# Optimization experiments

Hardware: AMD Instinct MI355X
Metric: run time of the kernel (lower is better)

## Reference

```python
import jax, jax.numpy as jnp
import numpy as np

B, H, S, D = 2, 16, 2048, 128
BS = 128  # block_size
NB = S // BS  # num_blocks
SPARSITY_PROB = 0.5


def setup_inputs() -> dict:
    key = jax.random.key(0)
    kq, kk, kv, km = jax.random.split(key, 4)
    query = jax.random.normal(kq, (B, H, S, D), dtype=jnp.float32)
    k_ = jax.random.normal(kk, (B, H, S, D), dtype=jnp.float32)
    v_ = jax.random.normal(kv, (B, H, S, D), dtype=jnp.float32)
    # block pattern: rand < sparsity_prob, diagonal forced True (causal=False)
    block_mask = jax.random.uniform(km, (NB, NB)) < SPARSITY_PROB
    block_mask = block_mask | jnp.eye(NB, dtype=bool)
    return {"query": query, "key": k_, "value": v_,
            "block_mask": block_mask, "block_size": BS}


def reference(query, key, value, block_mask, block_size):
    b, h, s, d = query.shape
    nb = s // block_size
    scale = 1.0 / jnp.sqrt(jnp.float32(d))
    # reshape into blocks: (b, h, nb, bs, d)
    qb = query.reshape(b, h, nb, block_size, d)
    kb = key.reshape(b, h, nb, block_size, d)
    vb = value.reshape(b, h, nb, block_size, d)
    # per-(i,j)-block scores: (b, h, i, j, q, k)
    scores = jnp.einsum('bhiqd,bhjkd->bhijqk', qb, kb) * scale
    # IMPORTANT: softmax is taken independently within each block (axis=-1),
    # matching the original's per-block (non-merged) softmax.
    attn = jax.nn.softmax(scores, axis=-1)
    # zero out inactive blocks, then sum contributions over j
    attn = attn * block_mask[None, None, :, :, None, None].astype(attn.dtype)
    out = jnp.einsum('bhijqk,bhjkd->bhiqd', attn, vb)
    return out.reshape(b, h, s, d)
```

## Files before the change

### kernel.cpp

```cpp
#include <hip/hip_runtime.h>
#include <stdint.h>

#define CBDIM 256
#define WBDIM 256
#define DBDIM 512

#if __has_builtin(__builtin_amdgcn_permlane32_swap) && \
    __has_builtin(__builtin_amdgcn_permlane16_swap)
#define HAVE_PERMLANE_SWAP 1
#else
#define HAVE_PERMLANE_SWAP 0
#endif

typedef __attribute__((ext_vector_type(8))) short short8;
typedef __attribute__((ext_vector_type(4))) float f32x4;

__device__ __forceinline__ unsigned f2bf(float f) {
    union { float f; unsigned u; } a; a.f = f;
    unsigned r = a.u + 0x7fffu + ((a.u >> 16) & 1u);
    return (r >> 16) & 0xffffu;
}
__device__ __forceinline__ float f4e(float4 v, int e) {
    return e == 0 ? v.x : e == 1 ? v.y : e == 2 ? v.z : v.w;
}
__device__ __forceinline__ unsigned u4e(uint4 v, int e) {
    return e == 0 ? v.x : e == 1 ? v.y : e == 2 ? v.z : v.w;
}
__device__ __forceinline__ uint2 shfl_u2(uint2 v, int src) {
    uint2 r;
    r.x = (unsigned)__shfl((int)v.x, src);
    r.y = (unsigned)__shfl((int)v.y, src);
    return r;
}
__device__ __forceinline__ bool detect_bf16(const void* p) {
    unsigned w = ((const unsigned*)p)[threadIdx.x & 63];
    unsigned lo = w & 0xffffu, ex = (lo >> 7) & 0xffu;
    bool pl = (lo == 0u) || (ex >= 0x68u && ex <= 0x86u);
    return __popcll(__ballot(pl)) >= 40;
}
__device__ __forceinline__ void gload_lds16(const void* g, void* l) {
    __builtin_amdgcn_global_load_lds(
        (const __attribute__((address_space(1))) void*)g,
        (__attribute__((address_space(3))) void*)l, 16, 0, 0);
}

__global__ __launch_bounds__(CBDIM)
void convert_kswz(const void* __restrict__ src, uint4* __restrict__ dst, int nIds)
{
    bool isBf = detect_bf16(src);
    int stride = gridDim.x * CBDIM;
    for (int id = blockIdx.x * CBDIM + threadIdx.x; id < nIds; id += stride) {
        int lid = id & 2047, tt = id >> 11;
        int r = lid >> 4, c = (lid & 15) ^ (r & 7);
        size_t eo = (size_t)tt * 16384 + (size_t)r * 128 + c * 8;
        uint4 w;
        if (isBf) {
            w = *(const uint4*)((const unsigned short*)src + eo);
        } else {
            const float* p = (const float*)src + eo;
            float4 f0 = *(const float4*)p, f1 = *(const float4*)(p + 4);
            w.x = f2bf(f0.x) | (f2bf(f0.y) << 16);
            w.y = f2bf(f0.z) | (f2bf(f0.w) << 16);
            w.z = f2bf(f1.x) | (f2bf(f1.y) << 16);
            w.w = f2bf(f1.z) | (f2bf(f1.w) << 16);
        }
        dst[id] = w;
    }
}

__global__ __launch_bounds__(CBDIM)
void convert_vt(const void* __restrict__ src, uint4* __restrict__ dst,
                const unsigned char* __restrict__ Mb, int* __restrict__ order)
{
    __shared__ unsigned short lv[16384];
    const int tid = threadIdx.x, t = blockIdx.x;
    bool isBf = detect_bf16(src);

    if (t == 0 && tid < 64) {
        int tt = tid;
        unsigned mu = ((const unsigned*)Mb)[tt];
        bool maskByte = (__ballot((mu & 0xFFFFFF00u) != 0u) != 0ull);
        int cnt = 0;
        if (tt < 16)
            for (int j = 0; j < 16; ++j) {
                bool a = maskByte ? (Mb[tt * 16 + j] != 0)
                                  : (((const int*)Mb)[tt * 16 + j] != 0);
                cnt += a ? 1 : 0;
            }
        int rank = 0;
        for (int j = 0; j < 16; ++j) {
            int cj = __shfl(cnt, j);
            if (cj > cnt || (cj == cnt && j < tt)) ++rank;
        }
        if (tt < 16) order[rank] = tt;
    }

    size_t ebase = (size_t)t * 16384;
    if (isBf) {
#pragma unroll
        for (int it = 0; it < 8; ++it) {
            int id = it * CBDIM + tid;
            *(uint4*)&lv[id * 8] = ((const uint4*)src)[ebase / 8 + id];
        }
    } else {
#pragma unroll
        for (int it = 0; it < 16; ++it) {
            int f = it * CBDIM + tid;
            float4 v = ((const float4*)src)[ebase / 4 + f];
            uint2 pk;
            pk.x = f2bf(v.x) | (f2bf(v.y) << 16);
            pk.y = f2bf(v.z) | (f2bf(v.w) << 16);
            *(uint2*)&lv[f * 4] = pk;
        }
    }
    __syncthreads();
#pragma unroll
    for (int it = 0; it < 8; ++it) {
        int id = it * CBDIM + tid;
        int d = id >> 4, c = (id & 15) ^ (d & 7);
        const unsigned short* col = &lv[(size_t)(c * 8) * 128 + d];
        uint4 w;
        w.x = col[0]   | ((unsigned)col[128] << 16);
        w.y = col[256] | ((unsigned)col[384] << 16);
        w.z = col[512] | ((unsigned)col[640] << 16);
        w.w = col[768] | ((unsigned)col[896] << 16);
        dst[(size_t)t * 2048 + id] = w;
    }
}

template<bool QF32>
__device__ __forceinline__ void attn_core(const void* Qv, const uint4* Kw,
                                          const uint4* Vt, unsigned actm,
                                          void* Ov, char* ldsK, char* ldsV,
                                          int bh, int i)
{
    constexpr int S = 2048, D = 128;
    const int tid  = threadIdx.x;
    const int lane = tid & 63;
    const int wv   = tid >> 6;
    const int quad = lane >> 4;
    const int l16  = lane & 15;

    const int qb0 = wv * 32;
    const size_t qrowbase = ((size_t)bh * S + (size_t)i * 128) * D;

    short8 qf[2][4];
#pragma unroll
    for (int nt = 0; nt < 2; ++nt) {
        int qrow = qb0 + nt * 16 + l16;
#pragma unroll
        for (int ks = 0; ks < 4; ++ks) {
            int dof = ks * 32 + quad * 8;
            if constexpr (QF32) {
                const float* qp = (const float*)Qv + qrowbase + (size_t)qrow * D + dof;
                float4 f0 = *(const float4*)qp;
                float4 f1 = *(const float4*)(qp + 4);
                short8 v;
                v[0] = (short)f2bf(f0.x); v[1] = (short)f2bf(f0.y);
                v[2] = (short)f2bf(f0.z); v[3] = (short)f2bf(f0.w);
                v[4] = (short)f2bf(f1.x); v[5] = (short)f2bf(f1.y);
                v[6] = (short)f2bf(f1.z); v[7] = (short)f2bf(f1.w);
                qf[nt][ks] = v;
            } else {
                qf[nt][ks] = *(const short8*)((const unsigned short*)Qv
                              + qrowbase + (size_t)qrow * D + dof);
            }
        }
    }

    f32x4 accO[2][8];
#pragma unroll
    for (int a = 0; a < 2; ++a)
#pragma unroll
        for (int b = 0; b < 8; ++b)
            accO[a][b] = (f32x4){0.f, 0.f, 0.f, 0.f};

    const float C2 = 0.08838834764831845f * 1.44269504088896f;

    auto STAGE = [&](const uint4* t, char* lds) {
#pragma unroll
        for (int it = 0; it < 8; ++it) {
            int id = it * WBDIM + tid;
            int lo = (it * WBDIM + wv * 64) * 16;
            gload_lds16(t + id, lds + lo);
        }
        asm volatile("" ::: "memory");
    };
    auto ktile = [&](int jj) { return Kw + (size_t)(bh * 16 + jj) * 2048; };
    auto vtile = [&](int jj) { return Vt + (size_t)(bh * 16 + jj) * 2048; };

    int j = (int)__builtin_ctz(actm);
    unsigned m = actm & (actm - 1);

    STAGE(ktile(j), ldsK);
    STAGE(vtile(j), ldsV);
    asm volatile("s_waitcnt vmcnt(8)" ::: "memory");
    __syncthreads();

    while (true) {
        int jn = m ? (int)__builtin_ctz(m) : -1;
        if (jn >= 0) m &= m - 1;

        f32x4 accS[2][8];
#pragma unroll
        for (int nt = 0; nt < 2; ++nt)
#pragma unroll
            for (int mt = 0; mt < 8; ++mt)
                accS[nt][mt] = (f32x4){0.f, 0.f, 0.f, 0.f};

#pragma unroll
        for (int mt = 0; mt < 8; ++mt) {
            int r = mt * 16 + l16;
            short8 kf[4];
#pragma unroll
            for (int ks = 0; ks < 4; ++ks) {
                int c = ks * 4 + quad;
                kf[ks] = *(const short8*)(ldsK + r * 256 + ((c ^ (r & 7)) << 4));
            }
            __builtin_amdgcn_s_setprio(1);
#pragma unroll
            for (int nt = 0; nt < 2; ++nt)
#pragma unroll
                for (int ks = 0; ks < 4; ++ks)
                    accS[nt][mt] = __builtin_amdgcn_mfma_f32_16x16x32_bf16(
                        kf[ks], qf[nt][ks], accS[nt][mt], 0, 0, 0);
            __builtin_amdgcn_s_setprio(0);
        }

        uint2 p2[2][8];
#pragma unroll
        for (int nt = 0; nt < 2; ++nt) {
            float ps[8];
#pragma unroll
            for (int mt = 0; mt < 8; ++mt) {
                f32x4 p;
#pragma unroll
                for (int rr = 0; rr < 4; ++rr)
                    p[rr] = exp2f(accS[nt][mt][rr] * C2);
                accS[nt][mt] = p;
                ps[mt] = (p[0] + p[1]) + (p[2] + p[3]);
            }
            float sum = ((ps[0] + ps[1]) + (ps[2] + ps[3]))
                      + ((ps[4] + ps[5]) + (ps[6] + ps[7]));
            sum += __shfl_xor(sum, 16);
            sum += __shfl_xor(sum, 32);
            float rinv = 1.0f / sum;
#pragma unroll
            for (int mt = 0; mt < 8; ++mt) {
                p2[nt][mt].x = f2bf(accS[nt][mt][0] * rinv)
                             | (f2bf(accS[nt][mt][1] * rinv) << 16);
                p2[nt][mt].y = f2bf(accS[nt][mt][2] * rinv)
                             | (f2bf(accS[nt][mt][3] * rinv) << 16);
            }
        }

        asm volatile("s_waitcnt vmcnt(0)" ::: "memory");
        __syncthreads();
        if (jn >= 0) STAGE(ktile(jn), ldsK);

#pragma unroll
        for (int ks = 0; ks < 4; ++ks) {
            short8 pf[2];
#pragma unroll
            for (int nt = 0; nt < 2; ++nt) {
#if HAVE_PERMLANE_SWAP
                unsigned ax = p2[nt][2 * ks + 0].x, ay = p2[nt][2 * ks + 0].y;
                unsigned bx = p2[nt][2 * ks + 1].x, by = p2[nt][2 * ks + 1].y;
                auto rx = __builtin_amdgcn_permlane32_swap(ax, bx, false, false);
                auto ry = __builtin_amdgcn_permlane32_swap(ay, by, false, false);
                auto sx = __builtin_amdgcn_permlane16_swap(rx[0], rx[1], false, false);
                auto sy = __builtin_amdgcn_permlane16_swap(ry[0], ry[1], false, false);
                union { uint4 u; short8 s; } w;
                w.u.x = sx[0]; w.u.y = sy[0]; w.u.z = sx[1]; w.u.w = sy[1];
                pf[nt] = w.s;
#else
                const int srcA = l16 + ((quad & 1) << 5);
                const int srcB = srcA + 16;
                const bool hiMs = (quad >> 1) != 0;
                uint2 a0 = shfl_u2(p2[nt][2 * ks + 0], srcA);
                uint2 a1 = shfl_u2(p2[nt][2 * ks + 1], srcA);
                uint2 b0 = shfl_u2(p2[nt][2 * ks + 0], srcB);
                uint2 b1 = shfl_u2(p2[nt][2 * ks + 1], srcB);
                uint2 lo, hi;
                lo.x = hiMs ? a1.x : a0.x;  lo.y = hiMs ? a1.y : a0.y;
                hi.x = hiMs ? b1.x : b0.x;  hi.y = hiMs ? b1.y : b0.y;
                union { uint4 u; short8 s; } w;
                w.u.x = lo.x; w.u.y = lo.y; w.u.z = hi.x; w.u.w = hi.y;
                pf[nt] = w.s;
#endif
            }
            __builtin_amdgcn_s_setprio(1);
#pragma unroll
            for (int dt = 0; dt < 8; ++dt) {
                int d = dt * 16 + l16;
                int c = ks * 4 + quad;
                short8 vf = *(const short8*)(ldsV + d * 256 + ((c ^ (d & 7)) << 4));
                accO[0][dt] = __builtin_amdgcn_mfma_f32_16x16x32_bf16(
                    pf[0], vf, accO[0][dt], 0, 0, 0);
                accO[1][dt] = __builtin_amdgcn_mfma_f32_16x16x32_bf16(
                    pf[1], vf, accO[1][dt], 0, 0, 0);
            }
            __builtin_amdgcn_s_setprio(0);
        }

        if (jn < 0) break;
        __syncthreads();
        STAGE(vtile(jn), ldsV);
        asm volatile("s_waitcnt vmcnt(8)" ::: "memory");
        __syncthreads();
        j = jn;
    }

#pragma unroll
    for (int mt = 0; mt < 2; ++mt)
#pragma unroll
        for (int rr = 0; rr < 4; ++rr) {
            int qrow = qb0 + mt * 16 + quad * 4 + rr;
#pragma unroll
            for (int nt = 0; nt < 8; ++nt) {
                size_t idx = qrowbase + (size_t)qrow * D + nt * 16 + l16;
                if constexpr (QF32)
                    ((float*)Ov)[idx] = accO[mt][nt][rr];
                else
                    ((unsigned short*)Ov)[idx] = (unsigned short)f2bf(accO[mt][nt][rr]);
            }
        }
}

__global__ __launch_bounds__(WBDIM, 2)
void attn_ws(const void* __restrict__ Q, const uint4* __restrict__ Kw,
             const uint4* __restrict__ Vt, const unsigned char* __restrict__ Mb,
             const int* __restrict__ order, void* __restrict__ O)
{
    __shared__ uint4 ldsK4[2048];
    __shared__ uint4 ldsV4[2048];
    int blk = blockIdx.x;
    int bh = ((blk >> 7) << 3) | (blk & 7);
    int slot = (blk >> 3) & 15;
    int i = order[(blk >> 8) ? (15 - slot) : slot];
    bool qBf = detect_bf16(Q);
    unsigned mu = ((const unsigned*)Mb)[threadIdx.x & 63];
    bool maskByte = (__ballot((mu & 0xFFFFFF00u) != 0u) != 0ull);
    unsigned actm = 0;
#pragma unroll
    for (int j = 0; j < 16; ++j) {
        bool a = maskByte ? (Mb[i * 16 + j] != 0)
                          : (((const int*)Mb)[i * 16 + j] != 0);
        actm |= (a ? 1u : 0u) << j;
    }
    if (qBf)
        attn_core<false>(Q, Kw, Vt, actm, O, (char*)ldsK4, (char*)ldsV4, bh, i);
    else
        attn_core<true>(Q, Kw, Vt, actm, O, (char*)ldsK4, (char*)ldsV4, bh, i);
}

template<bool QF32, bool KVF32>
__device__ __forceinline__ void attn_body(const void* Qv, const void* Kv,
                                          const void* Vv,
                                          const unsigned char* Mb, bool maskByte,
                                          void* Ov, char* ldsK, char* ldsV,
                                          int bh, int i)
{
    constexpr int S = 2048, D = 128;
    const int tid  = threadIdx.x;
    const int lane = tid & 63;
    const int wave = tid >> 6;
    const int quad = lane >> 4;
    const int l16  = lane & 15;

    const int qb0 = wave * 16;
    const size_t qrowbase = ((size_t)bh * S + (size_t)i * 128) * D;

    short8 qf[4];
    {
        int qrow = qb0 + l16;
#pragma unroll
        for (int ks = 0; ks < 4; ++ks) {
            int dof = ks * 32 + quad * 8;
            if constexpr (QF32) {
                const float* qp = (const float*)Qv + qrowbase + (size_t)qrow * D + dof;
                float4 f0 = *(const float4*)qp;
                float4 f1 = *(const float4*)(qp + 4);
                short8 v;
                v[0] = (short)f2bf(f0.x); v[1] = (short)f2bf(f0.y);
                v[2] = (short)f2bf(f0.z); v[3] = (short)f2bf(f0.w);
                v[4] = (short)f2bf(f1.x); v[5] = (short)f2bf(f1.y);
                v[6] = (short)f2bf(f1.z); v[7] = (short)f2bf(f1.w);
                qf[ks] = v;
            } else {
                qf[ks] = *(const short8*)((const unsigned short*)Qv
                          + qrowbase + (size_t)qrow * D + dof);
            }
        }
    }

    f32x4 accO[8];
#pragma unroll
    for (int b = 0; b < 8; ++b)
        accO[b] = (f32x4){0.f, 0.f, 0.f, 0.f};

    const float C2 = 0.08838834764831845f * 1.44269504088896f;
    const int srcA = l16 + ((quad & 1) << 5);
    const int srcB = srcA + 16;
    const bool hiMs = (quad >> 1) != 0;

    for (int j = 0; j < 16; ++j) {
        bool active = maskByte ? (Mb[i * 16 + j] != 0)
                               : (((const int*)Mb)[i * 16 + j] != 0);
        if (!active) continue;

        __syncthreads();
        const size_t kb = ((size_t)bh * S + (size_t)j * 128) * D;

        if constexpr (KVF32) {
#pragma unroll
            for (int it = 0; it < 8; ++it) {
                int f = it * DBDIM + tid;
                int r = f >> 5, c4 = f & 31;
                float4 v = ((const float4*)((const float*)Kv + kb))[f];
                uint2 pk;
                pk.x = f2bf(v.x) | (f2bf(v.y) << 16);
                pk.y = f2bf(v.z) | (f2bf(v.w) << 16);
                int ch = c4 >> 1;
                *(uint2*)(ldsK + r * 256 + ((ch ^ (r & 7)) << 4)
                          + ((c4 & 1) << 3)) = pk;
            }
        } else {
#pragma unroll
            for (int it = 0; it < 4; ++it) {
                int id = it * DBDIM + tid;
                int r = id >> 4, ch = id & 15;
                uint4 v = ((const uint4*)((const unsigned short*)Kv + kb))[id];
                *(uint4*)(ldsK + r * 256 + ((ch ^ (r & 7)) << 4)) = v;
            }
        }

        {
            int id = tid, pp = id & 31, dc = id >> 5;
            if constexpr (KVF32) {
                const float* vb = (const float*)Vv + kb + (size_t)(4 * pp) * D + dc * 8;
                float4 ra[4], rb[4];
#pragma unroll
                for (int r = 0; r < 4; ++r) {
                    ra[r] = *(const float4*)(vb + (size_t)r * D);
                    rb[r] = *(const float4*)(vb + (size_t)r * D + 4);
                }
#pragma unroll
                for (int e = 0; e < 8; ++e) {
                    float v0 = (e < 4) ? f4e(ra[0], e) : f4e(rb[0], e - 4);
                    float v1 = (e < 4) ? f4e(ra[1], e) : f4e(rb[1], e - 4);
                    float v2 = (e < 4) ? f4e(ra[2], e) : f4e(rb[2], e - 4);
                    float v3 = (e < 4) ? f4e(ra[3], e) : f4e(rb[3], e - 4);
                    uint2 pk;
                    pk.x = f2bf(v0) | (f2bf(v1) << 16);
                    pk.y = f2bf(v2) | (f2bf(v3) << 16);
                    int d = dc * 8 + e;
                    *(uint2*)(ldsV + d * 256 + (((pp >> 1) ^ (d & 7)) << 4)
                              + ((pp & 1) << 3)) = pk;
                }
            } else {
                const unsigned short* vb = (const unsigned short*)Vv + kb
                                           + (size_t)(4 * pp) * D + dc * 8;
                uint4 r0 = *(const uint4*)(vb);
                uint4 r1 = *(const uint4*)(vb + D);
                uint4 r2 = *(const uint4*)(vb + 2 * D);
                uint4 r3 = *(const uint4*)(vb + 3 * D);
#pragma unroll
                for (int e = 0; e < 8; ++e) {
                    unsigned h0 = u4e(r0, e >> 1), h1 = u4e(r1, e >> 1);
                    unsigned h2 = u4e(r2, e >> 1), h3 = u4e(r3, e >> 1);
                    if (e & 1) { h0 >>= 16; h1 >>= 16; h2 >>= 16; h3 >>= 16; }
                    uint2 pk;
                    pk.x = (h0 & 0xffffu) | (h1 << 16);
                    pk.y = (h2 & 0xffffu) | (h3 << 16);
                    int d = dc * 8 + e;
                    *(uint2*)(ldsV + d * 256 + (((pp >> 1) ^ (d & 7)) << 4)
                              + ((pp & 1) << 3)) = pk;
                }
            }
        }
        __syncthreads();

        f32x4 accS[8];
#pragma unroll
        for (int mt = 0; mt < 8; ++mt)
            accS[mt] = (f32x4){0.f, 0.f, 0.f, 0.f};

#pragma unroll
        for (int mt = 0; mt < 8; ++mt) {
            int r = mt * 16 + l16;
            short8 kf[4];
#pragma unroll
            for (int ks = 0; ks < 4; ++ks) {
                int c = ks * 4 + quad;
                kf[ks] = *(const short8*)(ldsK + r * 256 + ((c ^ (r & 7)) << 4));
            }
#pragma unroll
            for (int ks = 0; ks < 4; ++ks)
                accS[mt] = __builtin_amdgcn_mfma_f32_16x16x32_bf16(
                    kf[ks], qf[ks], accS[mt], 0, 0, 0);
        }

        float ps[8];
#pragma unroll
        for (int mt = 0; mt < 8; ++mt) {
            f32x4 p;
#pragma unroll
            for (int rr = 0; rr < 4; ++rr)
                p[rr] = exp2f(accS[mt][rr] * C2);
            accS[mt] = p;
            ps[mt] = (p[0] + p[1]) + (p[2] + p[3]);
        }
        float sum = ((ps[0] + ps[1]) + (ps[2] + ps[3]))
                  + ((ps[4] + ps[5]) + (ps[6] + ps[7]));
        sum += __shfl_xor(sum, 16);
        sum += __shfl_xor(sum, 32);
        float rinv = 1.0f / sum;

        uint2 p2[8];
#pragma unroll
        for (int mt = 0; mt < 8; ++mt) {
            p2[mt].x = f2bf(accS[mt][0] * rinv) | (f2bf(accS[mt][1] * rinv) << 16);
            p2[mt].y = f2bf(accS[mt][2] * rinv) | (f2bf(accS[mt][3] * rinv) << 16);
        }

#pragma unroll
        for (int ks = 0; ks < 4; ++ks) {
            short8 pf;
            {
                uint2 a0 = shfl_u2(p2[2 * ks + 0], srcA);
                uint2 a1 = shfl_u2(p2[2 * ks + 1], srcA);
                uint2 b0 = shfl_u2(p2[2 * ks + 0], srcB);
                uint2 b1 = shfl_u2(p2[2 * ks + 1], srcB);
                uint2 lo, hi;
                lo.x = hiMs ? a1.x : a0.x;  lo.y = hiMs ? a1.y : a0.y;
                hi.x = hiMs ? b1.x : b0.x;  hi.y = hiMs ? b1.y : b0.y;
                union { uint4 u; short8 s; } w;
                w.u.x = lo.x; w.u.y = lo.y; w.u.z = hi.x; w.u.w = hi.y;
                pf = w.s;
            }
#pragma unroll
            for (int dt = 0; dt < 8; ++dt) {
                int d = dt * 16 + l16;
                int c = ks * 4 + quad;
                short8 vf = *(const short8*)(ldsV + d * 256 + ((c ^ (d & 7)) << 4));
                accO[dt] = __builtin_amdgcn_mfma_f32_16x16x32_bf16(
                    pf, vf, accO[dt], 0, 0, 0);
            }
        }
    }

#pragma unroll
    for (int rr = 0; rr < 4; ++rr) {
        int qrow = qb0 + quad * 4 + rr;
#pragma unroll
        for (int dt = 0; dt < 8; ++dt) {
            size_t idx = qrowbase + (size_t)qrow * D + dt * 16 + l16;
            if constexpr (QF32)
                ((float*)Ov)[idx] = accO[dt][rr];
            else
                ((unsigned short*)Ov)[idx] = (unsigned short)f2bf(accO[dt][rr]);
        }
    }
}

__global__ __launch_bounds__(DBDIM, 4)
void attn_direct(const void* __restrict__ Q, const void* __restrict__ K,
                 const void* __restrict__ V,
                 const unsigned char* __restrict__ Mb, void* __restrict__ O)
{
    __shared__ uint4 ldsK4[2048];
    __shared__ uint4 ldsV4[2048];
    int blk = blockIdx.x;
    int bh = ((blk >> 7) << 3) | (blk & 7);
    int i  = (blk >> 3) & 15;
    bool qBf = detect_bf16(Q);
    unsigned mu = ((const unsigned*)Mb)[threadIdx.x & 63];
    bool maskByte = (__ballot((mu & 0xFFFFFF00u) != 0u) != 0ull);
    if (qBf)
        attn_body<false, false>(Q, K, V, Mb, maskByte, O,
                                (char*)ldsK4, (char*)ldsV4, bh, i);
    else
        attn_body<true, true>(Q, K, V, Mb, maskByte, O,
                              (char*)ldsK4, (char*)ldsV4, bh, i);
}

extern "C" void kernel_launch(void* const* d_in, const int* in_sizes, int n_in,
                              void* d_out, int out_size, void* d_ws, size_t ws_size,
                              hipStream_t stream) {
    const int NIDS = 512 * 2048;
    const size_t need = (size_t)NIDS * 16 * 2 + 256;
    if (ws_size >= need) {
        uint4* Kw = (uint4*)d_ws;
        uint4* Vt = Kw + NIDS;
        int* order = (int*)(Vt + NIDS);
        convert_kswz<<<1024, CBDIM, 0, stream>>>(d_in[1], Kw, NIDS);
        convert_vt<<<512, CBDIM, 0, stream>>>(d_in[2], Vt,
                                              (const unsigned char*)d_in[3], order);
        attn_ws<<<512, WBDIM, 0, stream>>>(d_in[0], Kw, Vt,
                                           (const unsigned char*)d_in[3],
                                           order, d_out);
    } else {
        attn_direct<<<512, DBDIM, 0, stream>>>(d_in[0], d_in[1], d_in[2],
                                               (const unsigned char*)d_in[3], d_out);
    }
}
```

Before: 213.3 us.

## Fuse K/V conversion kernels, relax barriers, use packed bf16 convert and permlane reductions

Merges the two preprocessing kernels into a single launch: the first 512 blocks transpose and convert V directly from registers without an LDS staging pass, and the rest convert K. In the attention loop, __syncthreads is replaced by raw s_barrier with explicit waitcnts, and the V restage no longer waits behind a second barrier. The softmax uses permlane swaps for its cross-lane reductions, a hardware reciprocal, and v_cvt_pk_bf16_f32 for packing. This removes a launch and an LDS round trip and trims ALU work, but the V-transpose writes are now scattered 8-byte stores, the rounding behaviour of the packed convert may differ, and the relaxed synchronisation has to stay correct.

```diff
diff --git a/kernel.cpp b/kernel.cpp
--- a/kernel.cpp
+++ b/kernel.cpp
@@ -20,6 +20,11 @@
     unsigned r = a.u + 0x7fffu + ((a.u >> 16) & 1u);
     return (r >> 16) & 0xffffu;
 }
+__device__ __forceinline__ unsigned cvtpk_bf16(float a, float b) {
+    unsigned r;
+    asm("v_cvt_pk_bf16_f32 %0, %1, %2" : "=v"(r) : "v"(a), "v"(b));
+    return r;
+}
 __device__ __forceinline__ float f4e(float4 v, int e) {
     return e == 0 ? v.x : e == 1 ? v.y : e == 2 ? v.z : v.w;
 }
@@ -32,6 +37,24 @@
     r.y = (unsigned)__shfl((int)v.y, src);
     return r;
 }
+__device__ __forceinline__ float xor16_f(float x, int lane) {
+#if HAVE_PERMLANE_SWAP
+    unsigned u = __float_as_uint(x);
+    auto r = __builtin_amdgcn_permlane16_swap(u, u, false, false);
+    return __uint_as_float((lane & 16) ? r[0] : r[1]);
+#else
+    return __shfl_xor(x, 16);
+#endif
+}
+__device__ __forceinline__ float xor32_f(float x, int lane) {
+#if HAVE_PERMLANE_SWAP
+    unsigned u = __float_as_uint(x);
+    auto r = __builtin_amdgcn_permlane32_swap(u, u, false, false);
+    return __uint_as_float((lane & 32) ? r[0] : r[1]);
+#else
+    return __shfl_xor(x, 32);
+#endif
+}
 __device__ __forceinline__ bool detect_bf16(const void* p) {
     unsigned w = ((const unsigned*)p)[threadIdx.x & 63];
     unsigned lo = w & 0xffffu, ex = (lo >> 7) & 0xffu;
@@ -45,86 +68,101 @@
 }
 
 __global__ __launch_bounds__(CBDIM)
-void convert_kswz(const void* __restrict__ src, uint4* __restrict__ dst, int nIds)
+void convert_fused(const void* __restrict__ Ksrc, const void* __restrict__ Vsrc,
+                   uint4* __restrict__ Kw, uint4* __restrict__ Vt,
+                   const unsigned char* __restrict__ Mb, int* __restrict__ order,
+                   int nIdsK)
 {
-    bool isBf = detect_bf16(src);
-    int stride = gridDim.x * CBDIM;
-    for (int id = blockIdx.x * CBDIM + threadIdx.x; id < nIds; id += stride) {
-        int lid = id & 2047, tt = id >> 11;
-        int r = lid >> 4, c = (lid & 15) ^ (r & 7);
-        size_t eo = (size_t)tt * 16384 + (size_t)r * 128 + c * 8;
-        uint4 w;
-        if (isBf) {
-            w = *(const uint4*)((const unsigned short*)src + eo);
-        } else {
-            const float* p = (const float*)src + eo;
-            float4 f0 = *(const float4*)p, f1 = *(const float4*)(p + 4);
-            w.x = f2bf(f0.x) | (f2bf(f0.y) << 16);
-            w.y = f2bf(f0.z) | (f2bf(f0.w) << 16);
-            w.z = f2bf(f1.x) | (f2bf(f1.y) << 16);
-            w.w = f2bf(f1.z) | (f2bf(f1.w) << 16);
-        }
-        dst[id] = w;
-    }
-}
-
-__global__ __launch_bounds__(CBDIM)
-void convert_vt(const void* __restrict__ src, uint4* __restrict__ dst,
-                const unsigned char* __restrict__ Mb, int* __restrict__ order)
-{
-    __shared__ unsigned short lv[16384];
-    const int tid = threadIdx.x, t = blockIdx.x;
-    bool isBf = detect_bf16(src);
-
-    if (t == 0 && tid < 64) {
-        int tt = tid;
-        unsigned mu = ((const unsigned*)Mb)[tt];
-        bool maskByte = (__ballot((mu & 0xFFFFFF00u) != 0u) != 0ull);
-        int cnt = 0;
-        if (tt < 16)
+    const int tid = threadIdx.x;
+    const int b = blockIdx.x;
+    if (b < 512) {
+        bool isBf = detect_bf16(Vsrc);
+        if (b == 0 && tid < 64) {
+            int tt = tid;
+            unsigned mu = ((const unsigned*)Mb)[tt];
+            bool maskByte = (__ballot((mu & 0xFFFFFF00u) != 0u) != 0ull);
+            int cnt = 0;
+            if (tt < 16)
+                for (int j = 0; j < 16; ++j) {
+                    bool a = maskByte ? (Mb[tt * 16 + j] != 0)
+                                      : (((const int*)Mb)[tt * 16 + j] != 0);
+                    cnt += a ? 1 : 0;
+                }
+            int rank = 0;
             for (int j = 0; j < 16; ++j) {
-                bool a = maskByte ? (Mb[tt * 16 + j] != 0)
-                                  : (((const int*)Mb)[tt * 16 + j] != 0);
-                cnt += a ? 1 : 0;
-            }
-        int rank = 0;
-        for (int j = 0; j < 16; ++j) {
-            int cj = __shfl(cnt, j);
-            if (cj > cnt || (cj == cnt && j < tt)) ++rank;
-        }
-        if (tt < 16) order[rank] = tt;
-    }
-
-    size_t ebase = (size_t)t * 16384;
-    if (isBf) {
-#pragma unroll
-        for (int it = 0; it < 8; ++it) {
-            int id = it * CBDIM + tid;
-            *(uint4*)&lv[id * 8] = ((const uint4*)src)[ebase / 8 + id];
+                int cj = __shfl(cnt, j);
+                if (cj > cnt || (cj == cnt && j < tt)) ++rank;
+            }
+            if (tt < 16) order[rank] = tt;
+        }
+        const size_t kb = (size_t)b * 16384;
+        char* base = (char*)(Vt + (size_t)b * 2048);
+#pragma unroll
+        for (int it = 0; it < 2; ++it) {
+            int id = it * CBDIM + tid, pp = id & 31, dc = id >> 5;
+            if (isBf) {
+                const unsigned short* vb = (const unsigned short*)Vsrc + kb
+                                           + (size_t)(4 * pp) * 128 + dc * 8;
+                uint4 r0 = *(const uint4*)(vb);
+                uint4 r1 = *(const uint4*)(vb + 128);
+                uint4 r2 = *(const uint4*)(vb + 256);
+                uint4 r3 = *(const uint4*)(vb + 384);
+#pragma unroll
+                for (int e = 0; e < 8; ++e) {
+                    unsigned h0 = u4e(r0, e >> 1), h1 = u4e(r1, e >> 1);
+                    unsigned h2 = u4e(r2, e >> 1), h3 = u4e(r3, e >> 1);
+                    if (e & 1) { h0 >>= 16; h1 >>= 16; h2 >>= 16; h3 >>= 16; }
+                    uint2 pk;
+                    pk.x = (h0 & 0xffffu) | (h1 << 16);
+                    pk.y = (h2 & 0xffffu) | (h3 << 16);
+                    int d = dc * 8 + e;
+                    *(uint2*)(base + d * 256 + (((pp >> 1) ^ (d & 7)) << 4)
+                              + ((pp & 1) << 3)) = pk;
+                }
+            } else {
+                const float* vb = (const float*)Vsrc + kb
+                                  + (size_t)(4 * pp) * 128 + dc * 8;
+                float4 ra[4], rb[4];
+#pragma unroll
+                for (int r = 0; r < 4; ++r) {
+                    ra[r] = *(const float4*)(vb + (size_t)r * 128);
+                    rb[r] = *(const float4*)(vb + (size_t)r * 128 + 4);
+                }
+#pragma unroll
+                for (int e = 0; e < 8; ++e) {
+                    float v0 = (e < 4) ? f4e(ra[0], e) : f4e(rb[0], e - 4);
+                    float v1 = (e < 4) ? f4e(ra[1], e) : f4e(rb[1], e - 4);
+                    float v2 = (e < 4) ? f4e(ra[2], e) : f4e(rb[2], e - 4);
+                    float v3 = (e < 4) ? f4e(ra[3], e) : f4e(rb[3], e - 4);
+                    uint2 pk;
+                    pk.x = f2bf(v0) | (f2bf(v1) << 16);
+                    pk.y = f2bf(v2) | (f2bf(v3) << 16);
+                    int d = dc * 8 + e;
+                    *(uint2*)(base + d * 256 + (((pp >> 1) ^ (d & 7)) << 4)
+                              + ((pp & 1) << 3)) = pk;
+                }
+            }
         }
     } else {
-#pragma unroll
-        for (int it = 0; it < 16; ++it) {
-            int f = it * CBDIM + tid;
-            float4 v = ((const float4*)src)[ebase / 4 + f];
-            uint2 pk;
-            pk.x = f2bf(v.x) | (f2bf(v.y) << 16);
-            pk.y = f2bf(v.z) | (f2bf(v.w) << 16);
-            *(uint2*)&lv[f * 4] = pk;
-        }
-    }
-    __syncthreads();
-#pragma unroll
-    for (int it = 0; it < 8; ++it) {
-        int id = it * CBDIM + tid;
-        int d = id >> 4, c = (id & 15) ^ (d & 7);
-        const unsigned short* col = &lv[(size_t)(c * 8) * 128 + d];
-        uint4 w;
-        w.x = col[0]   | ((unsigned)col[128] << 16);
-        w.y = col[256] | ((unsigned)col[384] << 16);
-        w.z = col[512] | ((unsigned)col[640] << 16);
-        w.w = col[768] | ((unsigned)col[896] << 16);
-        dst[(size_t)t * 2048 + id] = w;
+        bool isBf = detect_bf16(Ksrc);
+        int stride = ((int)gridDim.x - 512) * CBDIM;
+        for (int id = (b - 512) * CBDIM + tid; id < nIdsK; id += stride) {
+            int lid = id & 2047, tt = id >> 11;
+            int r = lid >> 4, c = (lid & 15) ^ (r & 7);
+            size_t eo = (size_t)tt * 16384 + (size_t)r * 128 + c * 8;
+            uint4 w;
+            if (isBf) {
+                w = *(const uint4*)((const unsigned short*)Ksrc + eo);
+            } else {
+                const float* p = (const float*)Ksrc + eo;
+                float4 f0 = *(const float4*)p, f1 = *(const float4*)(p + 4);
+                w.x = f2bf(f0.x) | (f2bf(f0.y) << 16);
+                w.y = f2bf(f0.z) | (f2bf(f0.w) << 16);
+                w.z = f2bf(f1.x) | (f2bf(f1.y) << 16);
+                w.w = f2bf(f1.z) | (f2bf(f1.w) << 16);
+            }
+            Kw[id] = w;
+        }
     }
 }
 
@@ -195,7 +233,7 @@
     STAGE(ktile(j), ldsK);
     STAGE(vtile(j), ldsV);
     asm volatile("s_waitcnt vmcnt(8)" ::: "memory");
-    __syncthreads();
+    asm volatile("s_barrier" ::: "memory");
 
     while (true) {
         int jn = m ? (int)__builtin_ctz(m) : -1;
@@ -242,20 +280,20 @@
             }
             float sum = ((ps[0] + ps[1]) + (ps[2] + ps[3]))
                       + ((ps[4] + ps[5]) + (ps[6] + ps[7]));
-            sum += __shfl_xor(sum, 16);
-            sum += __shfl_xor(sum, 32);
-            float rinv = 1.0f / sum;
+            sum += xor16_f(sum, lane);
+            sum += xor32_f(sum, lane);
+            float rinv = __builtin_amdgcn_rcpf(sum);
 #pragma unroll
             for (int mt = 0; mt < 8; ++mt) {
-                p2[nt][mt].x = f2bf(accS[nt][mt][0] * rinv)
-                             | (f2bf(accS[nt][mt][1] * rinv) << 16);
-                p2[nt][mt].y = f2bf(accS[nt][mt][2] * rinv)
-                             | (f2bf(accS[nt][mt][3] * rinv) << 16);
+                p2[nt][mt].x = cvtpk_bf16(accS[nt][mt][0] * rinv,
+                                          accS[nt][mt][1] * rinv);
+                p2[nt][mt].y = cvtpk_bf16(accS[nt][mt][2] * rinv,
+                                          accS[nt][mt][3] * rinv);
             }
         }
 
         asm volatile("s_waitcnt vmcnt(0)" ::: "memory");
-        __syncthreads();
+        asm volatile("s_barrier" ::: "memory");
         if (jn >= 0) STAGE(ktile(jn), ldsK);
 
 #pragma unroll
@@ -304,10 +342,9 @@
         }
 
         if (jn < 0) break;
-        __syncthreads();
+        asm volatile("s_waitcnt vmcnt(0)" ::: "memory");
+        asm volatile("s_barrier" ::: "memory");
         STAGE(vtile(jn), ldsV);
-        asm volatile("s_waitcnt vmcnt(8)" ::: "memory");
-        __syncthreads();
         j = jn;
     }
 
@@ -594,9 +631,9 @@
         uint4* Kw = (uint4*)d_ws;
         uint4* Vt = Kw + NIDS;
         int* order = (int*)(Vt + NIDS);
-        convert_kswz<<<1024, CBDIM, 0, stream>>>(d_in[1], Kw, NIDS);
-        convert_vt<<<512, CBDIM, 0, stream>>>(d_in[2], Vt,
-                                              (const unsigned char*)d_in[3], order);
+        convert_fused<<<1536, CBDIM, 0, stream>>>(d_in[1], d_in[2], Kw, Vt,
+                                                  (const unsigned char*)d_in[3],
+                                                  order, NIDS);
         attn_ws<<<512, WBDIM, 0, stream>>>(d_in[0], Kw, Vt,
                                            (const unsigned char*)d_in[3],
                                            order, d_out);
```

Result: faster. 197.5 us (-7.4%).
